# Performance work log

Hardware: AMD Instinct MI355X
Metric: run time of the kernel (lower is better)

Reference implementation:

```python
import jax, jax.numpy as jnp
import numpy as np

EMBED = 1024
HEADS = 16
HEAD_DIM = EMBED // HEADS


def setup_inputs() -> dict:
    key = jax.random.key(0)
    ks = jax.random.split(key, 12)
    B, S, E = 2, 2048, EMBED
    scale = 1.0 / np.sqrt(E)
    inp = {
        "query": jax.random.normal(ks[0], (B, S, E), jnp.float32),
        "key": jax.random.normal(ks[1], (B, S, E), jnp.float32),
        "value": jax.random.normal(ks[2], (B, S, E), jnp.float32),
        "Wq": jax.random.normal(ks[3], (E, E), jnp.float32) * scale,
        "bq": jax.random.normal(ks[4], (E,), jnp.float32) * 0.01,
        "Wk": jax.random.normal(ks[5], (E, E), jnp.float32) * scale,
        "bk": jax.random.normal(ks[6], (E,), jnp.float32) * 0.01,
        "Wv": jax.random.normal(ks[7], (E, E), jnp.float32) * scale,
        "bv": jax.random.normal(ks[8], (E,), jnp.float32) * 0.01,
        "Wo": jax.random.normal(ks[9], (E, E), jnp.float32) * scale,
        "bo": jax.random.normal(ks[10], (E,), jnp.float32) * 0.01,
    }
    return inp


def reference(query, key, value, Wq, bq, Wk, bk, Wv, bv, Wo, bo):
    B, Sq, E = query.shape
    Sk = key.shape[1]
    H, D = HEADS, HEAD_DIM
    # QKV projections (torch Linear: x @ W.T + b)
    q = (query @ Wq.T + bq).reshape(B, Sq, H, D)
    k = (key @ Wk.T + bk).reshape(B, Sk, H, D)
    v = (value @ Wv.T + bv).reshape(B, Sk, H, D)
    # energy: [B, H, Sq, Sk]; note scale = 1/sqrt(embed_size), not head_dim
    energy = jnp.einsum("bqhd,bkhd->bhqk", q, k)
    scale = jnp.asarray(E, energy.dtype) ** 0.5
    attn = jax.nn.softmax(energy / scale, axis=-1)
    out = jnp.einsum("bhqk,bkhd->bqhd", attn, v).reshape(B, Sq, E)
    # fc_out (dropout is identity at eval)
    return out @ Wo.T + bo
```

## Files before the change

### kernel.cpp

```cpp
#include <hip/hip_runtime.h>
#include <hip/hip_bf16.h>

typedef __hip_bfloat16 bf16;
typedef short frag8 __attribute__((ext_vector_type(8)));
typedef _Float16 half4 __attribute__((ext_vector_type(4)));
typedef float f32x4 __attribute__((ext_vector_type(4)));

typedef __attribute__((address_space(3))) void lds_void;
typedef __attribute__((address_space(1))) const void gbl_void;

__device__ __forceinline__ void gld16(const void* g, void* l) {
  __builtin_amdgcn_global_load_lds((gbl_void*)g, (lds_void*)l, 16, 0, 0);
}

__device__ __forceinline__ unsigned short f2bf(float f) {
  union { float f; unsigned u; } x; x.f = f;
  unsigned r = x.u + 0x7FFFu + ((x.u >> 16) & 1u);
  return (unsigned short)(r >> 16);
}

#define QSCALE 0.0450842200278f
#define MFIX 4.0f

struct CvtArgs {
  const float4* src[7];
  ushort4* dst[7];
  int n4[7];
};
__global__ __launch_bounds__(256) void cvt_all(CvtArgs a) {
  const int t = blockIdx.y;
  const int i = blockIdx.x * 256 + threadIdx.x;
  if (i >= a.n4[t]) return;
  float4 v = a.src[t][i];
  ushort4 o;
  o.x = f2bf(v.x); o.y = f2bf(v.y); o.z = f2bf(v.z); o.w = f2bf(v.w);
  a.dst[t][i] = o;
}

template<int J0>
__device__ __forceinline__ void mfma16(f32x4 (&acc)[8][4], const frag8 (&af)[8], const frag8 (&bf2)[2]) {
  __builtin_amdgcn_s_setprio(1);
  #pragma unroll
  for (int i = 0; i < 8; ++i) {
    #pragma unroll
    for (int j = 0; j < 2; ++j)
      acc[i][J0 + j] = __builtin_amdgcn_mfma_f32_16x16x32_bf16(af[i], bf2[j], acc[i][J0 + j], 0, 0, 0);
  }
  __builtin_amdgcn_s_setprio(0);
}

__global__ __launch_bounds__(512, 2)
void gemm_qkv256(const bf16* __restrict__ A0, const bf16* __restrict__ A1, const bf16* __restrict__ A2,
                 const bf16* __restrict__ W0, const bf16* __restrict__ W1, const bf16* __restrict__ W2,
                 const float* __restrict__ b0, const float* __restrict__ b1, const float* __restrict__ b2,
                 void* __restrict__ o0, void* __restrict__ o1, void* __restrict__ o2) {
  __shared__ __align__(16) bf16 As[2][16384];
  __shared__ __align__(16) bf16 Bs[2][16384];
  const int tid = threadIdx.x;
  const int wave = tid >> 6, lane = tid & 63, quad = lane >> 4, l16 = lane & 15;
  const int wm = wave >> 2, wn = wave & 3;
  const int bn = blockIdx.x, bm = blockIdx.y, z = blockIdx.z;

  const bf16* A = A0; const bf16* W = W0; const float* bias = b0; void* out = o0;
  if (z == 1) { A = A1; W = W1; bias = b1; out = o1; }
  else if (z == 2) { A = A2; W = W2; bias = b2; out = o2; }

  const bf16* Ab = A + (size_t)bm * 256 * 1024;
  const bf16* Wb = W + (size_t)bn * 256 * 1024;
  const int c0_ = tid & 3, r0_ = tid >> 2;
  const int gcp = ((c0_ ^ ((r0_ >> 1) & 3)) << 3);
  const int rc2 = (quad ^ ((l16 >> 1) & 3)) << 3;

  auto stage = [&](const bf16* src, int kt, int kh, bf16* dst) {
    #pragma unroll
    for (int is = 0; is < 2; ++is) {
      const int r = r0_ + is * 128;
      gld16(src + (size_t)r * 1024 + kt * 64 + kh * 32 + gcp,
            (void*)(dst + (is * 512 + tid) * 8));
    }
  };
  auto ldsA = [&](const bf16* ah, frag8 (&af)[8]) {
    #pragma unroll
    for (int i = 0; i < 8; ++i)
      af[i] = *(const frag8*)&ah[(wm * 128 + i * 16 + l16) * 32 + rc2];
  };
  auto ldsB2 = [&](const bf16* bh, int j0, frag8 (&bf2)[2]) {
    #pragma unroll
    for (int j = 0; j < 2; ++j)
      bf2[j] = *(const frag8*)&bh[(wn * 64 + (j0 + j) * 16 + l16) * 32 + rc2];
  };

  f32x4 acc[8][4];
  #pragma unroll
  for (int i = 0; i < 8; ++i)
    #pragma unroll
    for (int j = 0; j < 4; ++j)
      acc[i][j] = (f32x4){0.f, 0.f, 0.f, 0.f};

  stage(Ab, 0, 0, &As[0][0]);
  stage(Wb, 0, 0, &Bs[0][0]);
  stage(Ab, 0, 1, &As[0][8192]);
  stage(Wb, 0, 1, &Bs[0][8192]);
  asm volatile("s_waitcnt vmcnt(0)" ::: "memory");
  __builtin_amdgcn_s_barrier();

  #pragma unroll 2
  for (int t = 0; t < 15; ++t) {
    const int buf = t & 1, nb = buf ^ 1;
    const bf16* a0 = &As[buf][0];    const bf16* a1 = &As[buf][8192];
    const bf16* b0 = &Bs[buf][0];    const bf16* b1 = &Bs[buf][8192];
    frag8 af[8], bf2[2];

    ldsA(a0, af); ldsB2(b0, 0, bf2);
    stage(Ab, t + 1, 0, &As[nb][0]);
    __builtin_amdgcn_s_barrier();
    asm volatile("s_waitcnt lgkmcnt(0)" ::: "memory");
    mfma16<0>(acc, af, bf2);
    __builtin_amdgcn_s_barrier();

    ldsB2(b0, 2, bf2);
    stage(Wb, t + 1, 0, &Bs[nb][0]);
    asm volatile("s_waitcnt vmcnt(4)" ::: "memory");
    __builtin_amdgcn_s_barrier();
    asm volatile("s_waitcnt lgkmcnt(0)" ::: "memory");
    mfma16<2>(acc, af, bf2);
    __builtin_amdgcn_s_barrier();

    ldsA(a1, af); ldsB2(b1, 0, bf2);
    stage(Ab, t + 1, 1, &As[nb][8192]);
    __builtin_amdgcn_s_barrier();
    asm volatile("s_waitcnt lgkmcnt(0)" ::: "memory");
    mfma16<0>(acc, af, bf2);
    __builtin_amdgcn_s_barrier();

    ldsB2(b1, 2, bf2);
    stage(Wb, t + 1, 1, &Bs[nb][8192]);
    asm volatile("s_waitcnt vmcnt(4)" ::: "memory");
    __builtin_amdgcn_s_barrier();
    asm volatile("s_waitcnt lgkmcnt(0)" ::: "memory");
    mfma16<2>(acc, af, bf2);
    __builtin_amdgcn_s_barrier();
  }

  {
    const bf16* a0 = &As[1][0];    const bf16* a1 = &As[1][8192];
    const bf16* b0 = &Bs[1][0];    const bf16* b1 = &Bs[1][8192];
    frag8 af[8], bf2[2];
    ldsA(a0, af); ldsB2(b0, 0, bf2);
    __builtin_amdgcn_s_barrier();
    asm volatile("s_waitcnt lgkmcnt(0)" ::: "memory");
    mfma16<0>(acc, af, bf2);
    ldsB2(b0, 2, bf2);
    asm volatile("s_waitcnt vmcnt(0)" ::: "memory");
    __builtin_amdgcn_s_barrier();
    asm volatile("s_waitcnt lgkmcnt(0)" ::: "memory");
    mfma16<2>(acc, af, bf2);
    ldsA(a1, af); ldsB2(b1, 0, bf2);
    asm volatile("s_waitcnt lgkmcnt(0)" ::: "memory");
    mfma16<0>(acc, af, bf2);
    ldsB2(b1, 2, bf2);
    asm volatile("s_waitcnt lgkmcnt(0)" ::: "memory");
    mfma16<2>(acc, af, bf2);
  }

  #pragma unroll
  for (int j = 0; j < 4; ++j) {
    const int col = bn * 256 + wn * 64 + j * 16 + l16;
    const float bv = bias[col];
    #pragma unroll
    for (int i = 0; i < 8; ++i) {
      #pragma unroll
      for (int r = 0; r < 4; ++r) {
        const int row = bm * 256 + wm * 128 + i * 16 + quad * 4 + r;
        float v = acc[i][j][r] + bv;
        const int b = row >> 11, s = row & 2047;
        const int hh = col >> 6, d = col & 63;
        const size_t bh = (size_t)(b * 16 + hh);
        if (z == 0) {
          v *= QSCALE;
          ((bf16*)out)[(bh * 2048 + s) * 64 + d] = __float2bfloat16(v);
        } else if (z == 1) {
          const int rr = s & 127;
          const size_t addr = bh * 131072 + (size_t)(s >> 7) * 8192 + (size_t)rr * 64
                            + (size_t)(((d >> 3) ^ (rr & 7)) << 3) + (d & 7);
          ((bf16*)out)[addr] = __float2bfloat16(v);
        } else {
          const int kvl = s & 127;
          const size_t addr = bh * 131072 + (size_t)(s >> 7) * 8192 + (size_t)d * 128
                            + (size_t)((((kvl >> 2) ^ (d & 15)) << 2)) + (kvl & 3);
          ((_Float16*)out)[addr] = (_Float16)v;
        }
      }
    }
  }
}

template<int MODE>
__global__ __launch_bounds__(256)
void gemm_bt(const bf16* __restrict__ A0, const bf16* __restrict__ A1, const bf16* __restrict__ A2,
             const bf16* __restrict__ W0, const bf16* __restrict__ W1, const bf16* __restrict__ W2,
             const float* __restrict__ b0, const float* __restrict__ b1, const float* __restrict__ b2,
             void* __restrict__ o0, void* __restrict__ o1, void* __restrict__ o2) {
  constexpr int NK = 1024;
  constexpr int BN = (MODE == 1) ? 128 : 64;
  __shared__ __align__(16) bf16 As[2][128 * 32];
  __shared__ __align__(16) bf16 Bs[2][BN * 32];
  const int tid = threadIdx.x;
  const int wave = tid >> 6, lane = tid & 63, quad = lane >> 4, l16 = lane & 15;
  const int wm = wave >> 1, wn = wave & 1;
  const int bn = blockIdx.x, bm = blockIdx.y;

  const bf16* A = A0; const bf16* W = W0; const float* bias = b0; void* out = o0;
  int z = 0;
  if constexpr (MODE == 1) {
    z = blockIdx.z;
    if (z == 1) { A = A1; W = W1; bias = b1; out = o1; }
    else if (z == 2) { A = A2; W = W2; bias = b2; out = o2; }
  }

  const bf16* Ab = A + (size_t)bm * 128 * NK;
  const bf16* Wb = W + (size_t)bn * BN * NK;
  const int c0_ = tid & 3, r0_ = tid >> 2;
  const int rc = (quad ^ (l16 & 3)) << 3;

  auto stageA = [&](int k0, int buf) {
    #pragma unroll
    for (int is = 0; is < 2; ++is) {
      const int c = tid + is * 256;
      const int r = r0_ + is * 64;
      const int gc = (c0_ ^ (r & 3)) << 3;
      gld16(Ab + (size_t)r * NK + k0 + gc, (void*)(&As[buf][(size_t)c * 8]));
    }
  };
  auto stageW = [&](int k0, int buf) {
    if constexpr (MODE == 1) {
      #pragma unroll
      for (int is = 0; is < 2; ++is) {
        const int c = tid + is * 256;
        const int r = r0_ + is * 64;
        const int gc = (c0_ ^ (r & 3)) << 3;
        gld16(Wb + (size_t)r * NK + k0 + gc, (void*)(&Bs[buf][(size_t)c * 8]));
      }
    } else {
      const int r = r0_;
      const int gc = (c0_ ^ (r & 3)) << 3;
      gld16(Wb + (size_t)r * NK + k0 + gc, (void*)(&Bs[buf][(size_t)tid * 8]));
    }
  };

  if constexpr (MODE == 1) {
    f32x4 acc[4][4];
    #pragma unroll
    for (int i = 0; i < 4; ++i)
      #pragma unroll
      for (int j = 0; j < 4; ++j)
        acc[i][j] = (f32x4){0.f, 0.f, 0.f, 0.f};

    stageA(0, 0); stageW(0, 0);
    #pragma unroll 2
    for (int kt = 0; kt < 32; ++kt) {
      __syncthreads();
      if (kt < 31) { stageA((kt + 1) * 32, (kt + 1) & 1); stageW((kt + 1) * 32, (kt + 1) & 1); }
      const bf16* as_ = As[kt & 1];
      const bf16* bs_ = Bs[kt & 1];
      frag8 af[4], bfr[4];
      #pragma unroll
      for (int i = 0; i < 4; ++i)
        af[i] = *(const frag8*)&as_[(wm * 64 + i * 16 + l16) * 32 + rc];
      #pragma unroll
      for (int j = 0; j < 4; ++j)
        bfr[j] = *(const frag8*)&bs_[(wn * 64 + j * 16 + l16) * 32 + rc];
      #pragma unroll
      for (int i = 0; i < 4; ++i)
        #pragma unroll
        for (int j = 0; j < 4; ++j)
          acc[i][j] = __builtin_amdgcn_mfma_f32_16x16x32_bf16(af[i], bfr[j], acc[i][j], 0, 0, 0);
    }

    #pragma unroll
    for (int j = 0; j < 4; ++j) {
      const int col = bn * 128 + wn * 64 + j * 16 + l16;
      const float bv = bias[col];
      #pragma unroll
      for (int i = 0; i < 4; ++i) {
        #pragma unroll
        for (int r = 0; r < 4; ++r) {
          const int row = bm * 128 + wm * 64 + i * 16 + quad * 4 + r;
          float v = acc[i][j][r] + bv;
          const int b = row >> 11, s = row & 2047;
          const int hh = col >> 6, d = col & 63;
          const size_t bh = (size_t)(b * 16 + hh);
          if (z == 0) {
            v *= QSCALE;
            ((bf16*)out)[(bh * 2048 + s) * 64 + d] = __float2bfloat16(v);
          } else if (z == 1) {
            const int rr = s & 127;
            const size_t addr = bh * 131072 + (size_t)(s >> 7) * 8192 + (size_t)rr * 64
                              + (size_t)(((d >> 3) ^ (rr & 7)) << 3) + (d & 7);
            ((bf16*)out)[addr] = __float2bfloat16(v);
          } else {
            const int kvl = s & 127;
            const size_t addr = bh * 131072 + (size_t)(s >> 7) * 8192 + (size_t)d * 128
                              + (size_t)((((kvl >> 2) ^ (d & 15)) << 2)) + (kvl & 3);
            ((_Float16*)out)[addr] = (_Float16)v;
          }
        }
      }
    }
  } else {
    f32x4 acc[4][2];
    #pragma unroll
    for (int i = 0; i < 4; ++i)
      #pragma unroll
      for (int j = 0; j < 2; ++j)
        acc[i][j] = (f32x4){0.f, 0.f, 0.f, 0.f};

    stageA(0, 0); stageW(0, 0);
    #pragma unroll 2
    for (int kt = 0; kt < 32; ++kt) {
      __syncthreads();
      if (kt < 31) { stageA((kt + 1) * 32, (kt + 1) & 1); stageW((kt + 1) * 32, (kt + 1) & 1); }
      const bf16* as_ = As[kt & 1];
      const bf16* bs_ = Bs[kt & 1];
      frag8 af[4], bfr[2];
      #pragma unroll
      for (int i = 0; i < 4; ++i)
        af[i] = *(const frag8*)&as_[(wm * 64 + i * 16 + l16) * 32 + rc];
      #pragma unroll
      for (int j = 0; j < 2; ++j)
        bfr[j] = *(const frag8*)&bs_[(wn * 32 + j * 16 + l16) * 32 + rc];
      #pragma unroll
      for (int i = 0; i < 4; ++i)
        #pragma unroll
        for (int j = 0; j < 2; ++j)
          acc[i][j] = __builtin_amdgcn_mfma_f32_16x16x32_bf16(af[i], bfr[j], acc[i][j], 0, 0, 0);
    }

    #pragma unroll
    for (int j = 0; j < 2; ++j) {
      const int col = bn * 64 + wn * 32 + j * 16 + l16;
      const float bv = bias[col];
      #pragma unroll
      for (int i = 0; i < 4; ++i) {
        #pragma unroll
        for (int r = 0; r < 4; ++r) {
          const int row = bm * 128 + wm * 64 + i * 16 + quad * 4 + r;
          ((float*)out)[(size_t)row * 1024 + col] = acc[i][j][r] + bv;
        }
      }
    }
  }
}

__global__ __launch_bounds__(256)
void flash_attn(const bf16* __restrict__ Q, const bf16* __restrict__ K,
                const _Float16* __restrict__ Vt, bf16* __restrict__ ctx) {
  __shared__ __align__(16) bf16 Ks[2][128 * 64];
  __shared__ __align__(16) _Float16 Vs[2][64 * 128];
  const int tid = threadIdx.x;
  const int wave = tid >> 6, lane = tid & 63, quad = lane >> 4, l16 = lane & 15;
  const int bh = blockIdx.x, b = bh >> 4, h = bh & 15;
  const int q0 = blockIdx.y * 128 + wave * 32;
  const bf16* Qb = Q + (size_t)bh * 2048 * 64;
  const bf16* Kb = K + (size_t)bh * 131072;
  const _Float16* Vb = Vt + (size_t)bh * 131072;

  frag8 qf[2][2];
  #pragma unroll
  for (int qt = 0; qt < 2; ++qt)
    #pragma unroll
    for (int ks = 0; ks < 2; ++ks)
      qf[qt][ks] = *(const frag8*)(Qb + (size_t)(q0 + qt * 16 + l16) * 64 + ks * 32 + quad * 8);

  f32x4 rsv[2];
  f32x4 o[2][4];
  #pragma unroll
  for (int qt = 0; qt < 2; ++qt) {
    rsv[qt] = (f32x4){0.f, 0.f, 0.f, 0.f};
    #pragma unroll
    for (int dt = 0; dt < 4; ++dt)
      o[qt][dt] = (f32x4){0.f, 0.f, 0.f, 0.f};
  }

  const int xk = l16 & 7;

  auto stage = [&](int kt, int buf) {
    #pragma unroll
    for (int is = 0; is < 4; ++is) {
      const int c = tid + is * 256;
      gld16(Kb + (size_t)kt * 8192 + (size_t)c * 8, (void*)(&Ks[buf][(size_t)c * 8]));
      gld16(Vb + (size_t)kt * 8192 + (size_t)c * 8, (void*)(&Vs[buf][(size_t)c * 8]));
    }
  };

  stage(0, 0);
  #pragma unroll 2
  for (int kt = 0; kt < 16; ++kt) {
    __syncthreads();
    if (kt < 15) stage(kt + 1, (kt + 1) & 1);
    const bf16* ks_ = Ks[kt & 1];
    const _Float16* vs_ = Vs[kt & 1];

    f32x4 s[2][8];
    #pragma unroll
    for (int qt = 0; qt < 2; ++qt)
      #pragma unroll
      for (int jt = 0; jt < 8; ++jt)
        s[qt][jt] = (f32x4){-MFIX, -MFIX, -MFIX, -MFIX};
    #pragma unroll
    for (int ks = 0; ks < 2; ++ks) {
      frag8 kf[8];
      #pragma unroll
      for (int jt = 0; jt < 8; ++jt)
        kf[jt] = *(const frag8*)&ks_[(jt * 16 + l16) * 64 + (((ks * 4 + quad) ^ xk) << 3)];
      #pragma unroll
      for (int qt = 0; qt < 2; ++qt)
        #pragma unroll
        for (int jt = 0; jt < 8; ++jt)
          s[qt][jt] = __builtin_amdgcn_mfma_f32_16x16x32_bf16(kf[jt], qf[qt][ks], s[qt][jt], 0, 0, 0);
    }

    half4 pf[2][8];
    #pragma unroll
    for (int qt = 0; qt < 2; ++qt) {
      #pragma unroll
      for (int jt = 0; jt < 8; ++jt) {
        f32x4 p4;
        #pragma unroll
        for (int r = 0; r < 4; ++r)
          p4[r] = __builtin_amdgcn_exp2f(s[qt][jt][r]);
        rsv[qt] += p4;
        #pragma unroll
        for (int r = 0; r < 4; ++r)
          pf[qt][jt][r] = (_Float16)p4[r];
      }
    }

    #pragma unroll
    for (int jt = 0; jt < 8; ++jt) {
      half4 vf[4];
      #pragma unroll
      for (int dt = 0; dt < 4; ++dt)
        vf[dt] = *(const half4*)&vs_[(dt * 16 + l16) * 128 + (((jt * 4 + quad) ^ l16) << 2)];
      #pragma unroll
      for (int qt = 0; qt < 2; ++qt)
        #pragma unroll
        for (int dt = 0; dt < 4; ++dt)
          o[qt][dt] = __builtin_amdgcn_mfma_f32_16x16x16f16(vf[dt], pf[qt][jt], o[qt][dt], 0, 0, 0);
    }
  }

  #pragma unroll
  for (int qt = 0; qt < 2; ++qt) {
    float l = rsv[qt][0] + rsv[qt][1] + rsv[qt][2] + rsv[qt][3];
    l += __shfl_xor(l, 16, 64);
    l += __shfl_xor(l, 32, 64);
    const float inv = __builtin_amdgcn_rcpf(l);
    const int q = q0 + qt * 16 + l16;
    #pragma unroll
    for (int dt = 0; dt < 4; ++dt) {
      ushort4 w;
      w.x = f2bf(o[qt][dt][0] * inv);
      w.y = f2bf(o[qt][dt][1] * inv);
      w.z = f2bf(o[qt][dt][2] * inv);
      w.w = f2bf(o[qt][dt][3] * inv);
      const int d = dt * 16 + quad * 4;
      *(uint2*)&ctx[((size_t)(b * 2048 + q)) * 1024 + h * 64 + d] = *(uint2*)&w;
    }
  }
}

extern "C" void kernel_launch(void* const* d_in, const int* in_sizes, int n_in,
                              void* d_out, int out_size, void* d_ws, size_t ws_size,
                              hipStream_t stream) {
  const float* q_in = (const float*)d_in[0];
  const float* k_in = (const float*)d_in[1];
  const float* v_in = (const float*)d_in[2];
  const float* Wq = (const float*)d_in[3];
  const float* bq = (const float*)d_in[4];
  const float* Wk = (const float*)d_in[5];
  const float* bk = (const float*)d_in[6];
  const float* Wv = (const float*)d_in[7];
  const float* bv = (const float*)d_in[8];
  const float* Wo = (const float*)d_in[9];
  const float* bo = (const float*)d_in[10];

  char* ws = (char*)d_ws;
  const size_t MB = 1024 * 1024;
  bf16* Xq  = (bf16*)(ws + 0 * MB);
  bf16* Xk  = (bf16*)(ws + 8 * MB);
  bf16* Xv  = (bf16*)(ws + 16 * MB);
  bf16* Wqb = (bf16*)(ws + 24 * MB);
  bf16* Wkb = (bf16*)(ws + 26 * MB);
  bf16* Wvb = (bf16*)(ws + 28 * MB);
  bf16* Wob = (bf16*)(ws + 30 * MB);
  bf16* Qw  = (bf16*)(ws + 32 * MB);
  bf16* Kw  = (bf16*)(ws + 40 * MB);
  _Float16* Vtw = (_Float16*)(ws + 48 * MB);
  bf16* Ctx = (bf16*)(ws + 56 * MB);

  {
    CvtArgs a;
    a.src[0] = (const float4*)q_in; a.dst[0] = (ushort4*)Xq;  a.n4[0] = 4194304 / 4;
    a.src[1] = (const float4*)k_in; a.dst[1] = (ushort4*)Xk;  a.n4[1] = 4194304 / 4;
    a.src[2] = (const float4*)v_in; a.dst[2] = (ushort4*)Xv;  a.n4[2] = 4194304 / 4;
    a.src[3] = (const float4*)Wq;   a.dst[3] = (ushort4*)Wqb; a.n4[3] = 1048576 / 4;
    a.src[4] = (const float4*)Wk;   a.dst[4] = (ushort4*)Wkb; a.n4[4] = 1048576 / 4;
    a.src[5] = (const float4*)Wv;   a.dst[5] = (ushort4*)Wvb; a.n4[5] = 1048576 / 4;
    a.src[6] = (const float4*)Wo;   a.dst[6] = (ushort4*)Wob; a.n4[6] = 1048576 / 4;
    cvt_all<<<dim3(4096, 7), 256, 0, stream>>>(a);
  }

  gemm_qkv256<<<dim3(4, 16, 3), 512, 0, stream>>>(Xq, Xk, Xv, Wqb, Wkb, Wvb,
                                                  bq, bk, bv, Qw, Kw, (bf16*)Vtw);
  flash_attn<<<dim3(32, 16), 256, 0, stream>>>(Qw, Kw, Vtw, Ctx);
  gemm_bt<0><<<dim3(16, 32), 256, 0, stream>>>(Ctx, nullptr, nullptr, Wob, nullptr, nullptr,
                                               bo, nullptr, nullptr, d_out, nullptr, nullptr);
}
```

Before: 227.0 us.

## Split flash attention KV range across two wave groups with LDS merge

Flash attention now launches 512 threads per block. Each of two wave groups processes half of the KV sequence for the same 128 queries using 64-key sub-tiles, and partial outputs and row sums are merged through LDS at the end. The goal is to double the waves resident per block and hide latency better with the same grid, at the cost of a final reduction, extra synchronisation and a larger LDS footprint. It also adds s_setprio around the MFMA bursts, uses packed cvt_pkrtz for the fp16 probability conversion, and removes the unused MODE 1 path from gemm_bt.

```diff
diff --git a/kernel.cpp b/kernel.cpp
--- a/kernel.cpp
+++ b/kernel.cpp
@@ -4,6 +4,7 @@
 typedef __hip_bfloat16 bf16;
 typedef short frag8 __attribute__((ext_vector_type(8)));
 typedef _Float16 half4 __attribute__((ext_vector_type(4)));
+typedef __fp16 fp16x2 __attribute__((ext_vector_type(2)));
 typedef float f32x4 __attribute__((ext_vector_type(4)));
 
 typedef __attribute__((address_space(3))) void lds_void;
@@ -211,12 +212,6 @@
   const int bn = blockIdx.x, bm = blockIdx.y;
 
   const bf16* A = A0; const bf16* W = W0; const float* bias = b0; void* out = o0;
-  int z = 0;
-  if constexpr (MODE == 1) {
-    z = blockIdx.z;
-    if (z == 1) { A = A1; W = W1; bias = b1; out = o1; }
-    else if (z == 2) { A = A2; W = W2; bias = b2; out = o2; }
-  }
 
   const bf16* Ab = A + (size_t)bm * 128 * NK;
   const bf16* Wb = W + (size_t)bn * BN * NK;
@@ -233,135 +228,66 @@
     }
   };
   auto stageW = [&](int k0, int buf) {
-    if constexpr (MODE == 1) {
-      #pragma unroll
-      for (int is = 0; is < 2; ++is) {
-        const int c = tid + is * 256;
-        const int r = r0_ + is * 64;
-        const int gc = (c0_ ^ (r & 3)) << 3;
-        gld16(Wb + (size_t)r * NK + k0 + gc, (void*)(&Bs[buf][(size_t)c * 8]));
+    const int r = r0_;
+    const int gc = (c0_ ^ (r & 3)) << 3;
+    gld16(Wb + (size_t)r * NK + k0 + gc, (void*)(&Bs[buf][(size_t)tid * 8]));
+  };
+
+  f32x4 acc[4][2];
+  #pragma unroll
+  for (int i = 0; i < 4; ++i)
+    #pragma unroll
+    for (int j = 0; j < 2; ++j)
+      acc[i][j] = (f32x4){0.f, 0.f, 0.f, 0.f};
+
+  stageA(0, 0); stageW(0, 0);
+  #pragma unroll 2
+  for (int kt = 0; kt < 32; ++kt) {
+    __syncthreads();
+    if (kt < 31) { stageA((kt + 1) * 32, (kt + 1) & 1); stageW((kt + 1) * 32, (kt + 1) & 1); }
+    const bf16* as_ = As[kt & 1];
+    const bf16* bs_ = Bs[kt & 1];
+    frag8 af[4], bfr[2];
+    #pragma unroll
+    for (int i = 0; i < 4; ++i)
+      af[i] = *(const frag8*)&as_[(wm * 64 + i * 16 + l16) * 32 + rc];
+    #pragma unroll
+    for (int j = 0; j < 2; ++j)
+      bfr[j] = *(const frag8*)&bs_[(wn * 32 + j * 16 + l16) * 32 + rc];
+    #pragma unroll
+    for (int i = 0; i < 4; ++i)
+      #pragma unroll
+      for (int j = 0; j < 2; ++j)
+        acc[i][j] = __builtin_amdgcn_mfma_f32_16x16x32_bf16(af[i], bfr[j], acc[i][j], 0, 0, 0);
+  }
+
+  #pragma unroll
+  for (int j = 0; j < 2; ++j) {
+    const int col = bn * 64 + wn * 32 + j * 16 + l16;
+    const float bv = bias[col];
+    #pragma unroll
+    for (int i = 0; i < 4; ++i) {
+      #pragma unroll
+      for (int r = 0; r < 4; ++r) {
+        const int row = bm * 128 + wm * 64 + i * 16 + quad * 4 + r;
+        ((float*)out)[(size_t)row * 1024 + col] = acc[i][j][r] + bv;
       }
-    } else {
-      const int r = r0_;
-      const int gc = (c0_ ^ (r & 3)) << 3;
-      gld16(Wb + (size_t)r * NK + k0 + gc, (void*)(&Bs[buf][(size_t)tid * 8]));
-    }
-  };
-
-  if constexpr (MODE == 1) {
-    f32x4 acc[4][4];
-    #pragma unroll
-    for (int i = 0; i < 4; ++i)
-      #pragma unroll
-      for (int j = 0; j < 4; ++j)
-        acc[i][j] = (f32x4){0.f, 0.f, 0.f, 0.f};
-
-    stageA(0, 0); stageW(0, 0);
-    #pragma unroll 2
-    for (int kt = 0; kt < 32; ++kt) {
-      __syncthreads();
-      if (kt < 31) { stageA((kt + 1) * 32, (kt + 1) & 1); stageW((kt + 1) * 32, (kt + 1) & 1); }
-      const bf16* as_ = As[kt & 1];
-      const bf16* bs_ = Bs[kt & 1];
-      frag8 af[4], bfr[4];
-      #pragma unroll
-      for (int i = 0; i < 4; ++i)
-        af[i] = *(const frag8*)&as_[(wm * 64 + i * 16 + l16) * 32 + rc];
-      #pragma unroll
-      for (int j = 0; j < 4; ++j)
-        bfr[j] = *(const frag8*)&bs_[(wn * 64 + j * 16 + l16) * 32 + rc];
-      #pragma unroll
-      for (int i = 0; i < 4; ++i)
-        #pragma unroll
-        for (int j = 0; j < 4; ++j)
-          acc[i][j] = __builtin_amdgcn_mfma_f32_16x16x32_bf16(af[i], bfr[j], acc[i][j], 0, 0, 0);
-    }
-
-    #pragma unroll
-    for (int j = 0; j < 4; ++j) {
-      const int col = bn * 128 + wn * 64 + j * 16 + l16;
-      const float bv = bias[col];
-      #pragma unroll
-      for (int i = 0; i < 4; ++i) {
-        #pragma unroll
-        for (int r = 0; r < 4; ++r) {
-          const int row = bm * 128 + wm * 64 + i * 16 + quad * 4 + r;
-          float v = acc[i][j][r] + bv;
-          const int b = row >> 11, s = row & 2047;
-          const int hh = col >> 6, d = col & 63;
-          const size_t bh = (size_t)(b * 16 + hh);
-          if (z == 0) {
-            v *= QSCALE;
-            ((bf16*)out)[(bh * 2048 + s) * 64 + d] = __float2bfloat16(v);
-          } else if (z == 1) {
-            const int rr = s & 127;
-            const size_t addr = bh * 131072 + (size_t)(s >> 7) * 8192 + (size_t)rr * 64
-                              + (size_t)(((d >> 3) ^ (rr & 7)) << 3) + (d & 7);
-            ((bf16*)out)[addr] = __float2bfloat16(v);
-          } else {
-            const int kvl = s & 127;
-            const size_t addr = bh * 131072 + (size_t)(s >> 7) * 8192 + (size_t)d * 128
-                              + (size_t)((((kvl >> 2) ^ (d & 15)) << 2)) + (kvl & 3);
-            ((_Float16*)out)[addr] = (_Float16)v;
-          }
-        }
-      }
-    }
-  } else {
-    f32x4 acc[4][2];
-    #pragma unroll
-    for (int i = 0; i < 4; ++i)
-      #pragma unroll
-      for (int j = 0; j < 2; ++j)
-        acc[i][j] = (f32x4){0.f, 0.f, 0.f, 0.f};
-
-    stageA(0, 0); stageW(0, 0);
-    #pragma unroll 2
-    for (int kt = 0; kt < 32; ++kt) {
-      __syncthreads();
-      if (kt < 31) { stageA((kt + 1) * 32, (kt + 1) & 1); stageW((kt + 1) * 32, (kt + 1) & 1); }
-      const bf16* as_ = As[kt & 1];
-      const bf16* bs_ = Bs[kt & 1];
-      frag8 af[4], bfr[2];
-      #pragma unroll
-      for (int i = 0; i < 4; ++i)
-        af[i] = *(const frag8*)&as_[(wm * 64 + i * 16 + l16) * 32 + rc];
-      #pragma unroll
-      for (int j = 0; j < 2; ++j)
-        bfr[j] = *(const frag8*)&bs_[(wn * 32 + j * 16 + l16) * 32 + rc];
-      #pragma unroll
-      for (int i = 0; i < 4; ++i)
-        #pragma unroll
-        for (int j = 0; j < 2; ++j)
-          acc[i][j] = __builtin_amdgcn_mfma_f32_16x16x32_bf16(af[i], bfr[j], acc[i][j], 0, 0, 0);
-    }
-
-    #pragma unroll
-    for (int j = 0; j < 2; ++j) {
-      const int col = bn * 64 + wn * 32 + j * 16 + l16;
-      const float bv = bias[col];
-      #pragma unroll
-      for (int i = 0; i < 4; ++i) {
-        #pragma unroll
-        for (int r = 0; r < 4; ++r) {
-          const int row = bm * 128 + wm * 64 + i * 16 + quad * 4 + r;
-          ((float*)out)[(size_t)row * 1024 + col] = acc[i][j][r] + bv;
-        }
-      }
-    }
-  }
-}
-
-__global__ __launch_bounds__(256)
+    }
+  }
+}
+
+__global__ __launch_bounds__(512, 4)
 void flash_attn(const bf16* __restrict__ Q, const bf16* __restrict__ K,
                 const _Float16* __restrict__ Vt, bf16* __restrict__ ctx) {
-  __shared__ __align__(16) bf16 Ks[2][128 * 64];
-  __shared__ __align__(16) _Float16 Vs[2][64 * 128];
+  __shared__ __align__(16) char smem[65536];
+  bf16* Ks = (bf16*)smem;
+  _Float16* Vs = (_Float16*)(smem + 32768);
   const int tid = threadIdx.x;
   const int wave = tid >> 6, lane = tid & 63, quad = lane >> 4, l16 = lane & 15;
+  const int qg = wave & 3, kvg = wave >> 2;
   const int bh = blockIdx.x, b = bh >> 4, h = bh & 15;
-  const int q0 = blockIdx.y * 128 + wave * 32;
-  const bf16* Qb = Q + (size_t)bh * 2048 * 64;
+  const int q0 = blockIdx.y * 128 + qg * 32;
+  const bf16* Qb = Q + (size_t)bh * 131072;
   const bf16* Kb = K + (size_t)bh * 131072;
   const _Float16* Vb = Vt + (size_t)bh * 131072;
 
@@ -383,13 +309,16 @@
   }
 
   const int xk = l16 & 7;
+  const int vd = tid >> 3, vch = (tid & 7) << 3;
 
   auto stage = [&](int kt, int buf) {
     #pragma unroll
-    for (int is = 0; is < 4; ++is) {
-      const int c = tid + is * 256;
-      gld16(Kb + (size_t)kt * 8192 + (size_t)c * 8, (void*)(&Ks[buf][(size_t)c * 8]));
-      gld16(Vb + (size_t)kt * 8192 + (size_t)c * 8, (void*)(&Vs[buf][(size_t)c * 8]));
+    for (int s = 0; s < 2; ++s) {
+      const int g = s * 16 + kt;
+      const size_t kgo = (size_t)(g >> 1) * 8192 + (size_t)(g & 1) * 4096;
+      gld16(Kb + kgo + (size_t)tid * 8, (void*)(Ks + (s * 2 + buf) * 4096 + tid * 8));
+      const size_t vgo = (size_t)(g >> 1) * 8192 + (size_t)(g & 1) * 64;
+      gld16(Vb + vgo + (size_t)vd * 128 + vch, (void*)(Vs + (s * 2 + buf) * 4096 + tid * 8));
     }
   };
 
@@ -398,74 +327,100 @@
   for (int kt = 0; kt < 16; ++kt) {
     __syncthreads();
     if (kt < 15) stage(kt + 1, (kt + 1) & 1);
-    const bf16* ks_ = Ks[kt & 1];
-    const _Float16* vs_ = Vs[kt & 1];
-
-    f32x4 s[2][8];
+    const bf16* ks_ = Ks + (kvg * 2 + (kt & 1)) * 4096;
+    const _Float16* vs_ = Vs + (kvg * 2 + (kt & 1)) * 4096;
+
+    f32x4 s[2][4];
     #pragma unroll
     for (int qt = 0; qt < 2; ++qt)
       #pragma unroll
-      for (int jt = 0; jt < 8; ++jt)
+      for (int jt = 0; jt < 4; ++jt)
         s[qt][jt] = (f32x4){-MFIX, -MFIX, -MFIX, -MFIX};
     #pragma unroll
     for (int ks = 0; ks < 2; ++ks) {
-      frag8 kf[8];
-      #pragma unroll
-      for (int jt = 0; jt < 8; ++jt)
+      frag8 kf[4];
+      #pragma unroll
+      for (int jt = 0; jt < 4; ++jt)
         kf[jt] = *(const frag8*)&ks_[(jt * 16 + l16) * 64 + (((ks * 4 + quad) ^ xk) << 3)];
+      __builtin_amdgcn_s_setprio(1);
       #pragma unroll
       for (int qt = 0; qt < 2; ++qt)
         #pragma unroll
-        for (int jt = 0; jt < 8; ++jt)
+        for (int jt = 0; jt < 4; ++jt)
           s[qt][jt] = __builtin_amdgcn_mfma_f32_16x16x32_bf16(kf[jt], qf[qt][ks], s[qt][jt], 0, 0, 0);
-    }
-
-    half4 pf[2][8];
+      __builtin_amdgcn_s_setprio(0);
+    }
+
+    half4 pf[2][4];
     #pragma unroll
     for (int qt = 0; qt < 2; ++qt) {
       #pragma unroll
-      for (int jt = 0; jt < 8; ++jt) {
+      for (int jt = 0; jt < 4; ++jt) {
         f32x4 p4;
         #pragma unroll
         for (int r = 0; r < 4; ++r)
           p4[r] = __builtin_amdgcn_exp2f(s[qt][jt][r]);
         rsv[qt] += p4;
-        #pragma unroll
-        for (int r = 0; r < 4; ++r)
-          pf[qt][jt][r] = (_Float16)p4[r];
+        union { fp16x2 h2[2]; half4 h4; } u;
+        u.h2[0] = __builtin_amdgcn_cvt_pkrtz(p4[0], p4[1]);
+        u.h2[1] = __builtin_amdgcn_cvt_pkrtz(p4[2], p4[3]);
+        pf[qt][jt] = u.h4;
       }
     }
 
     #pragma unroll
-    for (int jt = 0; jt < 8; ++jt) {
+    for (int jt = 0; jt < 4; ++jt) {
       half4 vf[4];
       #pragma unroll
       for (int dt = 0; dt < 4; ++dt)
-        vf[dt] = *(const half4*)&vs_[(dt * 16 + l16) * 128 + (((jt * 4 + quad) ^ l16) << 2)];
+        vf[dt] = *(const half4*)&vs_[(dt * 16 + l16) * 64 + (((jt * 4 + quad) ^ l16) << 2)];
+      __builtin_amdgcn_s_setprio(1);
       #pragma unroll
       for (int qt = 0; qt < 2; ++qt)
         #pragma unroll
         for (int dt = 0; dt < 4; ++dt)
           o[qt][dt] = __builtin_amdgcn_mfma_f32_16x16x16f16(vf[dt], pf[qt][jt], o[qt][dt], 0, 0, 0);
-    }
-  }
-
-  #pragma unroll
-  for (int qt = 0; qt < 2; ++qt) {
-    float l = rsv[qt][0] + rsv[qt][1] + rsv[qt][2] + rsv[qt][3];
-    l += __shfl_xor(l, 16, 64);
-    l += __shfl_xor(l, 32, 64);
-    const float inv = __builtin_amdgcn_rcpf(l);
-    const int q = q0 + qt * 16 + l16;
-    #pragma unroll
-    for (int dt = 0; dt < 4; ++dt) {
-      ushort4 w;
-      w.x = f2bf(o[qt][dt][0] * inv);
-      w.y = f2bf(o[qt][dt][1] * inv);
-      w.z = f2bf(o[qt][dt][2] * inv);
-      w.w = f2bf(o[qt][dt][3] * inv);
-      const int d = dt * 16 + quad * 4;
-      *(uint2*)&ctx[((size_t)(b * 2048 + q)) * 1024 + h * 64 + d] = *(uint2*)&w;
+      __builtin_amdgcn_s_setprio(0);
+    }
+  }
+
+  __syncthreads();
+  float4* mo = (float4*)smem;
+  float*  ml = (float*)(smem + 32768);
+  const int mbase = (qg * 64 + lane) * 8;
+  if (kvg == 1) {
+    #pragma unroll
+    for (int qt = 0; qt < 2; ++qt)
+      #pragma unroll
+      for (int dt = 0; dt < 4; ++dt) {
+        const int i = qt * 4 + dt;
+        mo[mbase + (i ^ (lane & 7))] = (float4){o[qt][dt][0], o[qt][dt][1], o[qt][dt][2], o[qt][dt][3]};
+      }
+    ml[(qg * 64 + lane) * 2 + 0] = rsv[0][0] + rsv[0][1] + rsv[0][2] + rsv[0][3];
+    ml[(qg * 64 + lane) * 2 + 1] = rsv[1][0] + rsv[1][1] + rsv[1][2] + rsv[1][3];
+  }
+  __syncthreads();
+  if (kvg == 0) {
+    #pragma unroll
+    for (int qt = 0; qt < 2; ++qt) {
+      float l = rsv[qt][0] + rsv[qt][1] + rsv[qt][2] + rsv[qt][3]
+              + ml[(qg * 64 + lane) * 2 + qt];
+      l += __shfl_xor(l, 16, 64);
+      l += __shfl_xor(l, 32, 64);
+      const float inv = __builtin_amdgcn_rcpf(l);
+      const int q = q0 + qt * 16 + l16;
+      #pragma unroll
+      for (int dt = 0; dt < 4; ++dt) {
+        const int i = qt * 4 + dt;
+        const float4 po = mo[mbase + (i ^ (lane & 7))];
+        ushort4 w;
+        w.x = f2bf((o[qt][dt][0] + po.x) * inv);
+        w.y = f2bf((o[qt][dt][1] + po.y) * inv);
+        w.z = f2bf((o[qt][dt][2] + po.z) * inv);
+        w.w = f2bf((o[qt][dt][3] + po.w) * inv);
+        const int d = dt * 16 + quad * 4;
+        *(uint2*)&ctx[((size_t)(b * 2048 + q)) * 1024 + h * 64 + d] = *(uint2*)&w;
+      }
     }
   }
 }
@@ -513,7 +468,7 @@
 
   gemm_qkv256<<<dim3(4, 16, 3), 512, 0, stream>>>(Xq, Xk, Xv, Wqb, Wkb, Wvb,
                                                   bq, bk, bv, Qw, Kw, (bf16*)Vtw);
-  flash_attn<<<dim3(32, 16), 256, 0, stream>>>(Qw, Kw, Vtw, Ctx);
+  flash_attn<<<dim3(32, 16), 512, 0, stream>>>(Qw, Kw, Vtw, Ctx);
   gemm_bt<0><<<dim3(16, 32), 256, 0, stream>>>(Ctx, nullptr, nullptr, Wob, nullptr, nullptr,
                                                bo, nullptr, nullptr, d_out, nullptr, nullptr);
 }
```

Result: no change. 226.5 us (-0.2%).
